# Kernel tuning notes

Measured on AMD Instinct MI355X. Metric: run time of the kernel, lower is better.

## Reference

```python
import jax, jax.numpy as jnp
import numpy as np

BATCH = 4096
DIM = 512
TEMP = 0.5
EPS = 1e-8


def setup_inputs() -> dict:
    key = jax.random.key(0)
    k1, k2 = jax.random.split(key)
    z_i = jax.random.normal(k1, (BATCH, DIM), dtype=jnp.float32)
    z_j = jax.random.normal(k2, (BATCH, DIM), dtype=jnp.float32)
    return {"z_i": z_i, "z_j": z_j}


def reference(z_i, z_j):
    N = z_i.shape[0]
    temperature = jnp.asarray(TEMP, z_i.dtype)
    z = jnp.concatenate([z_i, z_j], axis=0)  # [2N, D]
    # cosine similarity = (x . y) / max(||x||*||y||, eps), as torch CosineSimilarity
    norms = jnp.sqrt(jnp.sum(z * z, axis=-1, keepdims=True))  # [2N, 1]
    dots = z @ z.T                                            # [2N, 2N]
    denom = jnp.maximum(norms * norms.T, EPS)
    sim = dots / denom / temperature                          # [2N, 2N]

    idx = jnp.arange(2 * N)
    # positive pair: offset +N / -N diagonals == partner index (i+N) mod 2N
    pos = sim[idx, (idx + N) % (2 * N)]                       # [2N]
    # CE with label 0 over logits [pos, negatives]: the full candidate set per
    # row is every sim entry except the self-diagonal (positive included once).
    masked = jnp.where(jnp.eye(2 * N, dtype=bool), -jnp.inf, sim)
    lse = jax.nn.logsumexp(masked, axis=1)                    # [2N]
    loss = jnp.sum(lse - pos) / (2 * N)
    return loss
```

## Files before the change

### kernel.cpp

```cpp
#include <hip/hip_runtime.h>


#define NROWS 8192
#define HALF_N 4096
#define KD 512
#define TILE 128
#define BK 128
#define NT (NROWS / TILE)

typedef unsigned char u8;
typedef __attribute__((ext_vector_type(4))) int i32x4;
typedef __attribute__((ext_vector_type(8))) int i32x8;
typedef __attribute__((ext_vector_type(4))) float f32x4;

__device__ inline void load16_to_lds(const u8* g, u8* l) {
  __builtin_amdgcn_global_load_lds((const __attribute__((address_space(1))) void*)g,
                                   (__attribute__((address_space(3))) void*)l,
                                   16, 0, 0);
}

__global__ __launch_bounds__(256) void nt_normalize(const float* __restrict__ zi,
                                                    const float* __restrict__ zj,
                                                    u8* __restrict__ zq,
                                                    float* __restrict__ rowsum,
                                                    float* __restrict__ possum,
                                                    float* __restrict__ out) {
  const int t = threadIdx.x;
  if (t < 4) rowsum[blockIdx.x * 4 + t] = 0.f;
  if (blockIdx.x == 0 && t == 4) { possum[0] = 0.f; out[0] = 0.f; }

  const int wave = t >> 6, lane = t & 63;
  const int row = blockIdx.x * 4 + wave;
  const float* src = (row < HALF_N) ? (zi + (size_t)row * KD)
                                    : (zj + (size_t)(row - HALF_N) * KD);
  const float4 v0 = ((const float4*)src)[lane * 2];
  const float4 v1 = ((const float4*)src)[lane * 2 + 1];
  float ss = v0.x * v0.x + v0.y * v0.y + v0.z * v0.z + v0.w * v0.w +
             v1.x * v1.x + v1.y * v1.y + v1.z * v1.z + v1.w * v1.w;
#pragma unroll
  for (int m = 1; m < 64; m <<= 1) ss += __shfl_xor(ss, m);
  const float inv = rsqrtf(ss);
  int lo = __builtin_amdgcn_cvt_pk_fp8_f32(v0.x * inv, v0.y * inv, 0, false);
  lo = __builtin_amdgcn_cvt_pk_fp8_f32(v0.z * inv, v0.w * inv, lo, true);
  int hi = __builtin_amdgcn_cvt_pk_fp8_f32(v1.x * inv, v1.y * inv, 0, false);
  hi = __builtin_amdgcn_cvt_pk_fp8_f32(v1.z * inv, v1.w * inv, hi, true);
  ((int2*)(zq + (size_t)row * KD))[lane] = make_int2(lo, hi);
}

__global__ __launch_bounds__(256) void nt_gemm(const u8* __restrict__ zq,
                                               float* __restrict__ rowsum,
                                               float* __restrict__ possum) {
  __shared__ __attribute__((aligned(16))) u8 lA[TILE * BK];
  __shared__ __attribute__((aligned(16))) u8 lB[TILE * BK];
  __shared__ float lrow[TILE];
  __shared__ float lcol[TILE];

  const int bid = blockIdx.x;
  int tm = (int)((float)(2 * NT + 1) * 0.5f -
                 sqrtf((float)(2 * NT + 1) * (float)(2 * NT + 1) * 0.25f - 2.0f * (float)bid));
  if (tm < 0) tm = 0;
  if (tm > NT - 1) tm = NT - 1;
  while ((tm + 1) * NT - ((tm + 1) * tm) / 2 <= bid) ++tm;
  while (tm * NT - (tm * (tm - 1)) / 2 > bid) --tm;
  const int tn = tm + (bid - (tm * NT - (tm * (tm - 1)) / 2));
  const bool diag = (tm == tn);
  const bool isPos = (tn - tm == 32);

  const int t = threadIdx.x;
  const int wave = t >> 6, lane = t & 63;
  const int wm = wave >> 1, wn = wave & 1;
  const int c16 = lane & 15, quad = lane >> 4;

  const int rowA = tm * TILE, rowB = tn * TILE;

  f32x4 acc[4][4] = {};

  const u8* Bt = diag ? lA : lB;
  const int q2 = quad * 2;

  for (int k0 = 0; k0 < KD; k0 += BK) {
    __syncthreads();
#pragma unroll
    for (int it = 0; it < 4; ++it) {
      const int chunk = it * 256 + t;
      const int r = chunk >> 3, cpos = chunk & 7;
      const int c = cpos ^ (r & 7);
      u8* dstA = &lA[(it * 256 + wave * 64) * 16];
      load16_to_lds(&zq[(size_t)(rowA + r) * KD + k0 + c * 16], dstA);
      if (!diag) {
        u8* dstB = &lB[(it * 256 + wave * 64) * 16];
        load16_to_lds(&zq[(size_t)(rowB + r) * KD + k0 + c * 16], dstB);
      }
    }
    __syncthreads();

    i32x8 bg[4];
#pragma unroll
    for (int ni = 0; ni < 4; ++ni) {
      const int rB = wn * 64 + ni * 16 + c16;
      const i32x4 bl = *(const i32x4*)&Bt[(rB * 8 + (q2 ^ (rB & 7))) * 16];
      const i32x4 bh = *(const i32x4*)&Bt[(rB * 8 + ((q2 + 1) ^ (rB & 7))) * 16];
      bg[ni] = (i32x8){bl[0], bl[1], bl[2], bl[3], bh[0], bh[1], bh[2], bh[3]};
    }
#pragma unroll
    for (int mi = 0; mi < 4; ++mi) {
      const int rA = wm * 64 + mi * 16 + c16;
      const i32x4 al = *(const i32x4*)&lA[(rA * 8 + (q2 ^ (rA & 7))) * 16];
      const i32x4 ah = *(const i32x4*)&lA[(rA * 8 + ((q2 + 1) ^ (rA & 7))) * 16];
      const i32x8 af = (i32x8){al[0], al[1], al[2], al[3], ah[0], ah[1], ah[2], ah[3]};
#pragma unroll
      for (int ni = 0; ni < 4; ++ni)
        acc[mi][ni] = __builtin_amdgcn_mfma_scale_f32_16x16x128_f8f6f4(
            af, bg[ni], acc[mi][ni],
            0, 0,
            0, 0x7F7F7F7F,
            0, 0x7F7F7F7F);
    }
  }

  const bool ownDiag = (quad == (c16 >> 2));
  const int rdiag = c16 & 3;

  if (isPos && wm == wn) {
    float p = 0.f;
    if (ownDiag) {
#pragma unroll
      for (int mi = 0; mi < 4; ++mi) p += acc[mi][mi][rdiag];
    }
#pragma unroll
    for (int m = 1; m < 64; m <<= 1) p += __shfl_xor(p, m);
    if (lane == 0) atomicAdd(possum, 4.0f * p);
  }

#pragma unroll
  for (int mi = 0; mi < 4; ++mi)
#pragma unroll
    for (int ni = 0; ni < 4; ++ni)
#pragma unroll
      for (int r = 0; r < 4; ++r)
        acc[mi][ni][r] = __expf(2.0f * acc[mi][ni][r]);

  if (diag && wm == wn && ownDiag) {
#pragma unroll
    for (int mi = 0; mi < 4; ++mi) acc[mi][mi][rdiag] = 0.f;
  }

  if (t < TILE) { lrow[t] = 0.f; lcol[t] = 0.f; }
  __syncthreads();

#pragma unroll
  for (int mi = 0; mi < 4; ++mi) {
#pragma unroll
    for (int r = 0; r < 4; ++r) {
      float e = acc[mi][0][r] + acc[mi][1][r] + acc[mi][2][r] + acc[mi][3][r];
      e += __shfl_xor(e, 1);
      e += __shfl_xor(e, 2);
      e += __shfl_xor(e, 4);
      e += __shfl_xor(e, 8);
      if (c16 == 0) atomicAdd(&lrow[wm * 64 + mi * 16 + quad * 4 + r], e);
    }
  }
  if (!diag) {
#pragma unroll
    for (int ni = 0; ni < 4; ++ni) {
      float g = 0.f;
#pragma unroll
      for (int mi = 0; mi < 4; ++mi)
#pragma unroll
        for (int r = 0; r < 4; ++r) g += acc[mi][ni][r];
      g += __shfl_xor(g, 16);
      g += __shfl_xor(g, 32);
      if (quad == 0) atomicAdd(&lcol[wn * 64 + ni * 16 + c16], g);
    }
  }
  __syncthreads();
  if (t < TILE) {
    atomicAdd(&rowsum[rowA + t], lrow[t]);
    if (!diag) atomicAdd(&rowsum[rowB + t], lcol[t]);
  }
}

__global__ __launch_bounds__(256) void nt_finalize(const float* __restrict__ rowsum,
                                                   const float* __restrict__ possum,
                                                   float* __restrict__ out) {
  const int t = threadIdx.x;
  const int i = blockIdx.x * 256 + t;
  float v = logf(rowsum[i]);
#pragma unroll
  for (int m = 1; m < 64; m <<= 1) v += __shfl_xor(v, m);
  __shared__ float bsum[4];
  if ((t & 63) == 0) bsum[t >> 6] = v;
  __syncthreads();
  if (t == 0) {
    float s = bsum[0] + bsum[1] + bsum[2] + bsum[3];
    if (blockIdx.x == 0) s -= possum[0];
    atomicAdd(out, s * (1.0f / NROWS));
  }
}

extern "C" void kernel_launch(void* const* d_in, const int* in_sizes, int n_in,
                              void* d_out, int out_size, void* d_ws, size_t ws_size,
                              hipStream_t stream) {
  const float* zi = (const float*)d_in[0];
  const float* zj = (const float*)d_in[1];
  float* out = (float*)d_out;

  u8* zq = (u8*)d_ws;
  float* rowsum = (float*)((char*)d_ws + (size_t)NROWS * KD);
  float* possum = rowsum + NROWS;

  nt_normalize<<<NROWS / 4, 256, 0, stream>>>(zi, zj, zq, rowsum, possum, out);
  nt_gemm<<<NT * (NT + 1) / 2, 256, 0, stream>>>(zq, rowsum, possum);
  nt_finalize<<<NROWS / 256, 256, 0, stream>>>(rowsum, possum, out);
}
```

Measured before the change: 109.8 us.

## Load GEMM fragments directly from global memory and remap blocks across XCDs

Staging through LDS with global_load_lds and the barriers around it is removed. Each lane now reads its MFMA A/B fragments straight from global memory, relying on L1/L2 caches for reuse. The block index is permuted so that consecutive triangular tiles land on the same XCD, which should improve L2 locality. Diagonal extraction and zeroing also become select loops so dynamic register indexing is avoided. The cost is redundant global traffic, because waves sharing rows each reload them, and LDS reuse is lost.

New measurement: 143.5 us. 1.31x slower.

```diff
diff --git a/kernel.cpp b/kernel.cpp
--- a/kernel.cpp
+++ b/kernel.cpp
@@ -7,17 +7,12 @@
 #define TILE 128
 #define BK 128
 #define NT (NROWS / TILE)
+#define NBLK (NT * (NT + 1) / 2)
 
 typedef unsigned char u8;
 typedef __attribute__((ext_vector_type(4))) int i32x4;
 typedef __attribute__((ext_vector_type(8))) int i32x8;
 typedef __attribute__((ext_vector_type(4))) float f32x4;
-
-__device__ inline void load16_to_lds(const u8* g, u8* l) {
-  __builtin_amdgcn_global_load_lds((const __attribute__((address_space(1))) void*)g,
-                                   (__attribute__((address_space(3))) void*)l,
-                                   16, 0, 0);
-}
 
 __global__ __launch_bounds__(256) void nt_normalize(const float* __restrict__ zi,
                                                     const float* __restrict__ zj,
@@ -50,12 +45,11 @@
 __global__ __launch_bounds__(256) void nt_gemm(const u8* __restrict__ zq,
                                                float* __restrict__ rowsum,
                                                float* __restrict__ possum) {
-  __shared__ __attribute__((aligned(16))) u8 lA[TILE * BK];
-  __shared__ __attribute__((aligned(16))) u8 lB[TILE * BK];
   __shared__ float lrow[TILE];
   __shared__ float lcol[TILE];
 
-  const int bid = blockIdx.x;
+  const int bid = (blockIdx.x & 7) * (NBLK / 8) + (blockIdx.x >> 3);
+
   int tm = (int)((float)(2 * NT + 1) * 0.5f -
                  sqrtf((float)(2 * NT + 1) * (float)(2 * NT + 1) * 0.25f - 2.0f * (float)bid));
   if (tm < 0) tm = 0;
@@ -71,42 +65,25 @@
   const int wm = wave >> 1, wn = wave & 1;
   const int c16 = lane & 15, quad = lane >> 4;
 
-  const int rowA = tm * TILE, rowB = tn * TILE;
+  const u8* baseA = zq + (size_t)(tm * TILE + wm * 64 + c16) * KD + quad * 32;
+  const u8* baseB = zq + (size_t)(tn * TILE + wn * 64 + c16) * KD + quad * 32;
 
   f32x4 acc[4][4] = {};
 
-  const u8* Bt = diag ? lA : lB;
-  const int q2 = quad * 2;
-
   for (int k0 = 0; k0 < KD; k0 += BK) {
-    __syncthreads();
-#pragma unroll
-    for (int it = 0; it < 4; ++it) {
-      const int chunk = it * 256 + t;
-      const int r = chunk >> 3, cpos = chunk & 7;
-      const int c = cpos ^ (r & 7);
-      u8* dstA = &lA[(it * 256 + wave * 64) * 16];
-      load16_to_lds(&zq[(size_t)(rowA + r) * KD + k0 + c * 16], dstA);
-      if (!diag) {
-        u8* dstB = &lB[(it * 256 + wave * 64) * 16];
-        load16_to_lds(&zq[(size_t)(rowB + r) * KD + k0 + c * 16], dstB);
-      }
-    }
-    __syncthreads();
-
     i32x8 bg[4];
 #pragma unroll
     for (int ni = 0; ni < 4; ++ni) {
-      const int rB = wn * 64 + ni * 16 + c16;
-      const i32x4 bl = *(const i32x4*)&Bt[(rB * 8 + (q2 ^ (rB & 7))) * 16];
-      const i32x4 bh = *(const i32x4*)&Bt[(rB * 8 + ((q2 + 1) ^ (rB & 7))) * 16];
+      const u8* pb = baseB + (size_t)(ni * 16) * KD + k0;
+      const i32x4 bl = *(const i32x4*)pb;
+      const i32x4 bh = *(const i32x4*)(pb + 16);
       bg[ni] = (i32x8){bl[0], bl[1], bl[2], bl[3], bh[0], bh[1], bh[2], bh[3]};
     }
 #pragma unroll
     for (int mi = 0; mi < 4; ++mi) {
-      const int rA = wm * 64 + mi * 16 + c16;
-      const i32x4 al = *(const i32x4*)&lA[(rA * 8 + (q2 ^ (rA & 7))) * 16];
-      const i32x4 ah = *(const i32x4*)&lA[(rA * 8 + ((q2 + 1) ^ (rA & 7))) * 16];
+      const u8* pa = baseA + (size_t)(mi * 16) * KD + k0;
+      const i32x4 al = *(const i32x4*)pa;
+      const i32x4 ah = *(const i32x4*)(pa + 16);
       const i32x8 af = (i32x8){al[0], al[1], al[2], al[3], ah[0], ah[1], ah[2], ah[3]};
 #pragma unroll
       for (int ni = 0; ni < 4; ++ni)
@@ -125,7 +102,10 @@
     float p = 0.f;
     if (ownDiag) {
 #pragma unroll
-      for (int mi = 0; mi < 4; ++mi) p += acc[mi][mi][rdiag];
+      for (int mi = 0; mi < 4; ++mi)
+#pragma unroll
+        for (int r = 0; r < 4; ++r)
+          p += (r == rdiag) ? acc[mi][mi][r] : 0.f;
     }
 #pragma unroll
     for (int m = 1; m < 64; m <<= 1) p += __shfl_xor(p, m);
@@ -142,7 +122,10 @@
 
   if (diag && wm == wn && ownDiag) {
 #pragma unroll
-    for (int mi = 0; mi < 4; ++mi) acc[mi][mi][rdiag] = 0.f;
+    for (int mi = 0; mi < 4; ++mi)
+#pragma unroll
+      for (int r = 0; r < 4; ++r)
+        acc[mi][mi][r] = (r == rdiag) ? 0.f : acc[mi][mi][r];
   }
 
   if (t < TILE) { lrow[t] = 0.f; lcol[t] = 0.f; }
@@ -175,8 +158,8 @@
   }
   __syncthreads();
   if (t < TILE) {
-    atomicAdd(&rowsum[rowA + t], lrow[t]);
-    if (!diag) atomicAdd(&rowsum[rowB + t], lcol[t]);
+    atomicAdd(&rowsum[tm * TILE + t], lrow[t]);
+    if (!diag) atomicAdd(&rowsum[tn * TILE + t], lcol[t]);
   }
 }
 
@@ -210,6 +193,6 @@
   float* possum = rowsum + NROWS;
 
   nt_normalize<<<NROWS / 4, 256, 0, stream>>>(zi, zj, zq, rowsum, possum, out);
-  nt_gemm<<<NT * (NT + 1) / 2, 256, 0, stream>>>(zq, rowsum, possum);
+  nt_gemm<<<NBLK, 256, 0, stream>>>(zq, rowsum, possum);
   nt_finalize<<<NROWS / 256, 256, 0, stream>>>(rowsum, possum, out);
 }
```
